# Performance work log

Measured on AMD Instinct MI355X. Metric: run time of the kernel, lower is better.

The kernel has to match this reference:

```python
import jax, jax.numpy as jnp
import numpy as np

N_NODES = 100000
N_EDGES = 1600000
F_IN = 256
F_OUT = 128


def setup_inputs() -> dict:
    key = jax.random.key(0)
    k_x, k_row, k_col, k_v, k_w = jax.random.split(key, 5)
    x = jax.random.normal(k_x, (N_NODES, F_IN), dtype=jnp.float32)
    row = jax.random.randint(k_row, (N_EDGES,), 0, N_NODES, dtype=jnp.int32)
    col = jax.random.randint(k_col, (N_EDGES,), 0, N_NODES, dtype=jnp.int32)
    vals = jax.random.uniform(k_v, (N_EDGES,), dtype=jnp.float32)
    # glorot init for weights_0 [F_IN, F_OUT]
    limit = np.sqrt(6.0 / (F_IN + F_OUT)).astype(np.float32)
    W = jax.random.uniform(k_w, (F_IN, F_OUT), minval=-limit, maxval=limit, dtype=jnp.float32)
    b = jnp.zeros((F_OUT,), dtype=jnp.float32)
    return {"x": x, "W": W, "b": b, "vals": vals, "row": row, "col": col}


def reference(x, W, b, vals, row, col):
    # dropout rate is 0.0 -> identity (tf.nn.dropout(x, keep_prob=1.0))
    pre_sup = x @ W  # [N, F_OUT] dense feature projection
    # SpMM: output[i] = sum_e (vals[e] * pre_sup[col[e]]) for edges with row[e] == i
    msgs = vals[:, None] * pre_sup[col]  # [E, F_OUT] gather + scale
    out = jax.ops.segment_sum(msgs, row, num_segments=N_NODES)  # scatter-add
    return jax.nn.relu(out + b)
```

## Files before the change

### kernel.cpp

```cpp
#include <hip/hip_runtime.h>
#include <hip/hip_bf16.h>

#define N_NODES 100000
#define N_EDGES 1600000
#define F_IN 256
#define F_OUT 128

#define N_BINS 128
#define RPB 782
#define L1_BLOCKS 256
#define L1_THREADS 512
#define L1_EDGES (N_EDGES / L1_BLOCKS)
#define CNT_SIZE (N_BINS * L1_BLOCKS)

typedef __attribute__((ext_vector_type(8))) short short8;
typedef __attribute__((ext_vector_type(4))) float f32x4;
typedef __attribute__((ext_vector_type(2))) float f32x2;
typedef __attribute__((ext_vector_type(2))) unsigned int uint2v;

static __device__ __forceinline__ unsigned short bf16b(float f) {
    __hip_bfloat16 h = __float2bfloat16(f);
    return *reinterpret_cast<unsigned short*>(&h);
}

__global__ void wprep_kernel(const float* __restrict__ W, unsigned short* __restrict__ Wsw) {
    int idx = blockIdx.x * 256 + threadIdx.x;
    int e  = idx & 7;
    int col = (idx >> 3) & 127;
    int kk = (idx >> 10) & 3;
    int ks = idx >> 12;
    int k = ks * 32 + kk * 8 + e;
    Wsw[idx] = bf16b(W[k * 128 + col]);
}

__global__ __launch_bounds__(64) void gemm_kernel(const float* __restrict__ x,
                                                  const unsigned short* __restrict__ Wsw,
                                                  unsigned short* __restrict__ preb) {
    __shared__ char sx[16384];
    const int lane = threadIdx.x;
    const int m0 = blockIdx.x * 16;
    const int l15 = lane & 15;
    const int kk = lane >> 4;

#pragma unroll
    for (int j = 0; j < 16; ++j) {
        const char* gsrc = reinterpret_cast<const char*>(x + (size_t)(m0 + j) * F_IN)
                         + ((lane ^ j) << 4);
        __builtin_amdgcn_global_load_lds(
            (const __attribute__((address_space(1))) void*)gsrc,
            (__attribute__((address_space(3))) void*)(sx + j * 1024),
            16, 0, 0);
    }
    __syncthreads();

    f32x4 acc[8];
#pragma unroll
    for (int i = 0; i < 8; ++i) acc[i] = (f32x4){0.f, 0.f, 0.f, 0.f};

    const char* swb = sx + l15 * 1024;
    const int sw = l15 << 4;
#pragma unroll
    for (int ks = 0; ks < 8; ++ks) {
        const int cb = ks * 128 + kk * 32;
        float4 fa = *reinterpret_cast<const float4*>(swb + ((cb) ^ sw));
        float4 fb = *reinterpret_cast<const float4*>(swb + ((cb + 16) ^ sw));
        short8 a;
        a[0] = (short)bf16b(fa.x); a[1] = (short)bf16b(fa.y);
        a[2] = (short)bf16b(fa.z); a[3] = (short)bf16b(fa.w);
        a[4] = (short)bf16b(fb.x); a[5] = (short)bf16b(fb.y);
        a[6] = (short)bf16b(fb.z); a[7] = (short)bf16b(fb.w);
        const short8* wv = reinterpret_cast<const short8*>(Wsw) + ((ks * 4 + kk) * 128 + l15);
#pragma unroll
        for (int nf = 0; nf < 8; ++nf) {
            short8 b = wv[nf * 16];
            acc[nf] = __builtin_amdgcn_mfma_f32_16x16x32_bf16(a, b, acc[nf], 0, 0, 0);
        }
    }

    const int rbase = m0 + (lane >> 4) * 4;
#pragma unroll
    for (int nf = 0; nf < 8; ++nf) {
        int cc = nf * 16 + l15;
#pragma unroll
        for (int reg = 0; reg < 4; ++reg) {
            preb[(long)(rbase + reg) * F_OUT + cc] = bf16b(acc[nf][reg]);
        }
    }
}

__global__ __launch_bounds__(L1_THREADS) void passA_kernel(const int* __restrict__ row,
                                                           int* __restrict__ cnt) {
    __shared__ int h[N_BINS];
    if (threadIdx.x < N_BINS) h[threadIdx.x] = 0;
    __syncthreads();
    const int g = blockIdx.x;
    const int base = g * L1_EDGES;
    for (int i = threadIdx.x; i < L1_EDGES; i += L1_THREADS) {
        int r = __builtin_nontemporal_load(row + base + i);
        atomicAdd(&h[r / RPB], 1);
    }
    __syncthreads();
    if (threadIdx.x < N_BINS)
        cnt[threadIdx.x * L1_BLOCKS + g] = h[threadIdx.x];
}

__global__ void scan32768_kernel(const int* __restrict__ cnt, int* __restrict__ off) {
    __shared__ int tmp[1024];
    int t = threadIdx.x;
    const int4* c4 = reinterpret_cast<const int4*>(cnt);
    int sum = 0;
#pragma unroll
    for (int j = 0; j < 8; ++j) {
        int4 v = c4[t * 8 + j];
        sum += v.x + v.y + v.z + v.w;
    }
    tmp[t] = sum;
    __syncthreads();
#pragma unroll
    for (int o = 1; o < 1024; o <<= 1) {
        int u = (t >= o) ? tmp[t - o] : 0;
        __syncthreads();
        tmp[t] += u;
        __syncthreads();
    }
    int base = tmp[t] - sum;
#pragma unroll
    for (int j = 0; j < 8; ++j) {
        int4 v = c4[t * 8 + j];
        off[t * 32 + j * 4 + 0] = base; base += v.x;
        off[t * 32 + j * 4 + 1] = base; base += v.y;
        off[t * 32 + j * 4 + 2] = base; base += v.z;
        off[t * 32 + j * 4 + 3] = base; base += v.w;
    }
    if (t == 1023) off[CNT_SIZE] = base;
}

__global__ __launch_bounds__(L1_THREADS) void passB_kernel(const int* __restrict__ row,
                                                           const int* __restrict__ col,
                                                           const float* __restrict__ vals,
                                                           const int* __restrict__ off,
                                                           unsigned* __restrict__ packed,
                                                           unsigned short* __restrict__ valh) {
    __shared__ int cur[N_BINS];
    const int g = blockIdx.x;
    if (threadIdx.x < N_BINS) cur[threadIdx.x] = off[threadIdx.x * L1_BLOCKS + g];
    __syncthreads();
    const int base = g * L1_EDGES;
    for (int i = threadIdx.x; i < L1_EDGES; i += L1_THREADS) {
        int e = base + i;
        int r = __builtin_nontemporal_load(row + e);
        int c = __builtin_nontemporal_load(col + e);
        float v = __builtin_nontemporal_load(vals + e);
        int bin = r / RPB;
        int lr = r - bin * RPB;
        int pos = atomicAdd(&cur[bin], 1);
        packed[pos] = (unsigned)c | ((unsigned)lr << 17);
        valh[pos] = bf16b(v);
    }
}

__global__ __launch_bounds__(1024) void csr_fused_kernel(const unsigned* __restrict__ packed,
                                                         const unsigned short* __restrict__ valh,
                                                         const int* __restrict__ off,
                                                         int* __restrict__ row_start,
                                                         uint2v* __restrict__ edges) {
    __shared__ int tmp[1024];
    const int b = blockIdx.x;
    const int t = threadIdx.x;
    const int rbase = b * RPB;
    const int nrows = min(RPB, N_NODES - rbase);
    const int lo = off[b * L1_BLOCKS];
    const int hi = off[(b + 1) * L1_BLOCKS];

    tmp[t] = 0;
    __syncthreads();
    for (int i = lo + t; i < hi; i += 1024)
        atomicAdd(&tmp[packed[i] >> 17], 1);
    __syncthreads();

    int d = tmp[t];
#pragma unroll
    for (int o = 1; o < 1024; o <<= 1) {
        int u = (t >= o) ? tmp[t - o] : 0;
        __syncthreads();
        tmp[t] += u;
        __syncthreads();
    }
    int excl = lo + tmp[t] - d;
    if (t < nrows) row_start[rbase + t] = excl;
    if (b == N_BINS - 1 && t == 0) row_start[N_NODES] = N_EDGES;
    tmp[t] = excl;
    __syncthreads();

    for (int i = lo + t; i < hi; i += 1024) {
        unsigned p = packed[i];
        unsigned short vh = valh[i];
        int pos = atomicAdd(&tmp[p >> 17], 1);
        edges[pos] = (uint2v){p & 0x1FFFFu, ((unsigned)vh) << 16};
    }
}

__global__ __launch_bounds__(256) void spmm_csr_kernel(
    const unsigned short* __restrict__ preb, const int* __restrict__ row_start,
    const uint2v* __restrict__ edges, const float* __restrict__ bias,
    float* __restrict__ out) {
    const int lane = threadIdx.x & 63;
    const int r = blockIdx.x * 4 + (threadIdx.x >> 6);
    const int s = row_start[r];
    const int t = row_start[r + 1];
    const int n = t - s;
    float a0 = 0.f, a1 = 0.f;

    const char* pb = reinterpret_cast<const char*>(preb);
    const unsigned laneoff = (unsigned)(lane << 2);

    uint2v ev = (uint2v){0u, 0u};
    if (lane < n) ev = edges[s + lane];
    const int nn = n < 64 ? n : 64;
    for (int j0 = 0; j0 < nn; j0 += 8) {
#pragma unroll
        for (int jj = 0; jj < 8; ++jj) {
            int j = j0 + jj;
            unsigned c = (unsigned)__builtin_amdgcn_readlane((int)ev.x, j);
            float v = __uint_as_float((unsigned)__builtin_amdgcn_readlane((int)ev.y, j));
            const char* pbase = pb + ((size_t)c << 8);
            unsigned g = *reinterpret_cast<const unsigned*>(pbase + laneoff);
            a0 += v * __uint_as_float(g << 16);
            a1 += v * __uint_as_float(g & 0xFFFF0000u);
        }
    }
    for (int e = s + 64; e < t; ++e) {
        uint2v cv = edges[e];
        float v = __uint_as_float(cv.y);
        const char* pbase = pb + ((size_t)cv.x << 8);
        unsigned g = *reinterpret_cast<const unsigned*>(pbase + laneoff);
        a0 += v * __uint_as_float(g << 16);
        a1 += v * __uint_as_float(g & 0xFFFF0000u);
    }

    float2 bb = *reinterpret_cast<const float2*>(bias + lane * 2);
    f32x2 o;
    o.x = fmaxf(a0 + bb.x, 0.f);
    o.y = fmaxf(a1 + bb.y, 0.f);
    __builtin_nontemporal_store(o, reinterpret_cast<f32x2*>(out + (size_t)r * F_OUT + lane * 2));
}

extern "C" void kernel_launch(void* const* d_in, const int* in_sizes, int n_in,
                              void* d_out, int out_size, void* d_ws, size_t ws_size,
                              hipStream_t stream) {
    const float* x    = (const float*)d_in[0];
    const float* W    = (const float*)d_in[1];
    const float* b    = (const float*)d_in[2];
    const float* vals = (const float*)d_in[3];
    const int*   row  = (const int*)d_in[4];
    const int*   col  = (const int*)d_in[5];
    float* out = (float*)d_out;

    char* ws = (char*)d_ws;
    unsigned short* preb      = (unsigned short*)(ws);
    unsigned short* Wsw       = (unsigned short*)(ws + 25600000);
    int*            row_start = (int*)(ws + 25665536);
    int*            cnt       = (int*)(ws + 26469664);
    int*            off       = (int*)(ws + 26600736);
    unsigned*       packed    = (unsigned*)(ws + 26731904);
    unsigned short* valh      = (unsigned short*)(ws + 33131904);
    uint2v*         edges     = (uint2v*)(ws + 36331904);

    wprep_kernel<<<128, 256, 0, stream>>>(W, Wsw);
    gemm_kernel<<<N_NODES / 16, 64, 0, stream>>>(x, Wsw, preb);

    passA_kernel<<<L1_BLOCKS, L1_THREADS, 0, stream>>>(row, cnt);
    scan32768_kernel<<<1, 1024, 0, stream>>>(cnt, off);
    passB_kernel<<<L1_BLOCKS, L1_THREADS, 0, stream>>>(row, col, vals, off, packed, valh);

    csr_fused_kernel<<<N_BINS, 1024, 0, stream>>>(packed, valh, off, row_start, edges);

    spmm_csr_kernel<<<N_NODES / 4, 256, 0, stream>>>(preb, row_start, edges, b, out);
}
```

Baseline: 160.6 us.

## Fuse weight prep with histogram and GEMM with scatter into shared launches

Merges the weight bf16 swizzle with the row histogram pass in one launch, and the edge scatter pass with the dense GEMM in another, selecting work by block index. This cuts the kernel count from seven to five and lets the memory-bound scatter overlap with the compute-bound GEMM. Histogram and scatter blocks shrink to 64 threads and their count doubles to 512, so the count array and scan double in size (65536 entries). Atomic contention per block drops, but the single-block scan now handles twice the data and the workspace offsets are repacked.

```diff
diff --git a/kernel.cpp b/kernel.cpp
--- a/kernel.cpp
+++ b/kernel.cpp
@@ -8,8 +8,7 @@
 
 #define N_BINS 128
 #define RPB 782
-#define L1_BLOCKS 256
-#define L1_THREADS 512
+#define L1_BLOCKS 512
 #define L1_EDGES (N_EDGES / L1_BLOCKS)
 #define CNT_SIZE (N_BINS * L1_BLOCKS)
 
@@ -23,22 +22,102 @@
     return *reinterpret_cast<unsigned short*>(&h);
 }
 
-__global__ void wprep_kernel(const float* __restrict__ W, unsigned short* __restrict__ Wsw) {
-    int idx = blockIdx.x * 256 + threadIdx.x;
-    int e  = idx & 7;
-    int col = (idx >> 3) & 127;
-    int kk = (idx >> 10) & 3;
-    int ks = idx >> 12;
-    int k = ks * 32 + kk * 8 + e;
-    Wsw[idx] = bf16b(W[k * 128 + col]);
-}
-
-__global__ __launch_bounds__(64) void gemm_kernel(const float* __restrict__ x,
-                                                  const unsigned short* __restrict__ Wsw,
-                                                  unsigned short* __restrict__ preb) {
-    __shared__ char sx[16384];
-    const int lane = threadIdx.x;
-    const int m0 = blockIdx.x * 16;
+__global__ __launch_bounds__(64) void fuseA_kernel(const float* __restrict__ W,
+                                                   unsigned short* __restrict__ Wsw,
+                                                   const int* __restrict__ row,
+                                                   int* __restrict__ cnt) {
+    const int t = threadIdx.x;
+    if (blockIdx.x < 512) {
+        int idx = blockIdx.x * 64 + t;
+        int e  = idx & 7;
+        int col = (idx >> 3) & 127;
+        int kk = (idx >> 10) & 3;
+        int ks = idx >> 12;
+        int k = ks * 32 + kk * 8 + e;
+        Wsw[idx] = bf16b(W[k * 128 + col]);
+    } else {
+        __shared__ int h[N_BINS];
+        h[t] = 0; h[t + 64] = 0;
+        __syncthreads();
+        const int g = blockIdx.x - 512;
+        const int base = g * L1_EDGES;
+        for (int i = t; i < L1_EDGES; i += 64) {
+            int r = __builtin_nontemporal_load(row + base + i);
+            atomicAdd(&h[r / RPB], 1);
+        }
+        __syncthreads();
+        cnt[t * L1_BLOCKS + g] = h[t];
+        cnt[(t + 64) * L1_BLOCKS + g] = h[t + 64];
+    }
+}
+
+__global__ void scan65536_kernel(const int* __restrict__ cnt, int* __restrict__ off) {
+    __shared__ int tmp[1024];
+    int t = threadIdx.x;
+    const int4* c4 = reinterpret_cast<const int4*>(cnt);
+    int sum = 0;
+#pragma unroll
+    for (int j = 0; j < 16; ++j) {
+        int4 v = c4[t * 16 + j];
+        sum += v.x + v.y + v.z + v.w;
+    }
+    tmp[t] = sum;
+    __syncthreads();
+#pragma unroll
+    for (int o = 1; o < 1024; o <<= 1) {
+        int u = (t >= o) ? tmp[t - o] : 0;
+        __syncthreads();
+        tmp[t] += u;
+        __syncthreads();
+    }
+    int base = tmp[t] - sum;
+#pragma unroll
+    for (int j = 0; j < 16; ++j) {
+        int4 v = c4[t * 16 + j];
+        off[t * 64 + j * 4 + 0] = base; base += v.x;
+        off[t * 64 + j * 4 + 1] = base; base += v.y;
+        off[t * 64 + j * 4 + 2] = base; base += v.z;
+        off[t * 64 + j * 4 + 3] = base; base += v.w;
+    }
+    if (t == 1023) off[CNT_SIZE] = base;
+}
+
+__global__ __launch_bounds__(64) void fuseB_kernel(const int* __restrict__ row,
+                                                   const int* __restrict__ col,
+                                                   const float* __restrict__ vals,
+                                                   const int* __restrict__ off,
+                                                   unsigned* __restrict__ packed,
+                                                   unsigned short* __restrict__ valh,
+                                                   const float* __restrict__ x,
+                                                   const unsigned short* __restrict__ Wsw,
+                                                   unsigned short* __restrict__ preb) {
+    __shared__ char smem[16384];
+    const int t = threadIdx.x;
+
+    if (blockIdx.x < 512) {
+        int* cur = reinterpret_cast<int*>(smem);
+        const int g = blockIdx.x;
+        cur[t] = off[t * L1_BLOCKS + g];
+        cur[t + 64] = off[(t + 64) * L1_BLOCKS + g];
+        __syncthreads();
+        const int base = g * L1_EDGES;
+        for (int i = t; i < L1_EDGES; i += 64) {
+            int e = base + i;
+            int r = __builtin_nontemporal_load(row + e);
+            int c = __builtin_nontemporal_load(col + e);
+            float v = __builtin_nontemporal_load(vals + e);
+            int bin = r / RPB;
+            int lr = r - bin * RPB;
+            int pos = atomicAdd(&cur[bin], 1);
+            packed[pos] = (unsigned)c | ((unsigned)lr << 17);
+            valh[pos] = bf16b(v);
+        }
+        return;
+    }
+
+    char* sx = smem;
+    const int lane = t;
+    const int m0 = (blockIdx.x - 512) * 16;
     const int l15 = lane & 15;
     const int kk = lane >> 4;
 
@@ -85,77 +164,6 @@
         for (int reg = 0; reg < 4; ++reg) {
             preb[(long)(rbase + reg) * F_OUT + cc] = bf16b(acc[nf][reg]);
         }
-    }
-}
-
-__global__ __launch_bounds__(L1_THREADS) void passA_kernel(const int* __restrict__ row,
-                                                           int* __restrict__ cnt) {
-    __shared__ int h[N_BINS];
-    if (threadIdx.x < N_BINS) h[threadIdx.x] = 0;
-    __syncthreads();
-    const int g = blockIdx.x;
-    const int base = g * L1_EDGES;
-    for (int i = threadIdx.x; i < L1_EDGES; i += L1_THREADS) {
-        int r = __builtin_nontemporal_load(row + base + i);
-        atomicAdd(&h[r / RPB], 1);
-    }
-    __syncthreads();
-    if (threadIdx.x < N_BINS)
-        cnt[threadIdx.x * L1_BLOCKS + g] = h[threadIdx.x];
-}
-
-__global__ void scan32768_kernel(const int* __restrict__ cnt, int* __restrict__ off) {
-    __shared__ int tmp[1024];
-    int t = threadIdx.x;
-    const int4* c4 = reinterpret_cast<const int4*>(cnt);
-    int sum = 0;
-#pragma unroll
-    for (int j = 0; j < 8; ++j) {
-        int4 v = c4[t * 8 + j];
-        sum += v.x + v.y + v.z + v.w;
-    }
-    tmp[t] = sum;
-    __syncthreads();
-#pragma unroll
-    for (int o = 1; o < 1024; o <<= 1) {
-        int u = (t >= o) ? tmp[t - o] : 0;
-        __syncthreads();
-        tmp[t] += u;
-        __syncthreads();
-    }
-    int base = tmp[t] - sum;
-#pragma unroll
-    for (int j = 0; j < 8; ++j) {
-        int4 v = c4[t * 8 + j];
-        off[t * 32 + j * 4 + 0] = base; base += v.x;
-        off[t * 32 + j * 4 + 1] = base; base += v.y;
-        off[t * 32 + j * 4 + 2] = base; base += v.z;
-        off[t * 32 + j * 4 + 3] = base; base += v.w;
-    }
-    if (t == 1023) off[CNT_SIZE] = base;
-}
-
-__global__ __launch_bounds__(L1_THREADS) void passB_kernel(const int* __restrict__ row,
-                                                           const int* __restrict__ col,
-                                                           const float* __restrict__ vals,
-                                                           const int* __restrict__ off,
-                                                           unsigned* __restrict__ packed,
-                                                           unsigned short* __restrict__ valh) {
-    __shared__ int cur[N_BINS];
-    const int g = blockIdx.x;
-    if (threadIdx.x < N_BINS) cur[threadIdx.x] = off[threadIdx.x * L1_BLOCKS + g];
-    __syncthreads();
-    const int base = g * L1_EDGES;
-    for (int i = threadIdx.x; i < L1_EDGES; i += L1_THREADS) {
-        int e = base + i;
-        int r = __builtin_nontemporal_load(row + e);
-        int c = __builtin_nontemporal_load(col + e);
-        float v = __builtin_nontemporal_load(vals + e);
-        int bin = r / RPB;
-        int lr = r - bin * RPB;
-        int pos = atomicAdd(&cur[bin], 1);
-        packed[pos] = (unsigned)c | ((unsigned)lr << 17);
-        valh[pos] = bf16b(v);
     }
 }
 
@@ -260,20 +268,16 @@
     unsigned short* preb      = (unsigned short*)(ws);
     unsigned short* Wsw       = (unsigned short*)(ws + 25600000);
     int*            row_start = (int*)(ws + 25665536);
-    int*            cnt       = (int*)(ws + 26469664);
-    int*            off       = (int*)(ws + 26600736);
-    unsigned*       packed    = (unsigned*)(ws + 26731904);
-    unsigned short* valh      = (unsigned short*)(ws + 33131904);
-    uint2v*         edges     = (uint2v*)(ws + 36331904);
-
-    wprep_kernel<<<128, 256, 0, stream>>>(W, Wsw);
-    gemm_kernel<<<N_NODES / 16, 64, 0, stream>>>(x, Wsw, preb);
-
-    passA_kernel<<<L1_BLOCKS, L1_THREADS, 0, stream>>>(row, cnt);
-    scan32768_kernel<<<1, 1024, 0, stream>>>(cnt, off);
-    passB_kernel<<<L1_BLOCKS, L1_THREADS, 0, stream>>>(row, col, vals, off, packed, valh);
-
+    int*            cnt       = (int*)(ws + 26065552);
+    int*            off       = (int*)(ws + 26327696);
+    unsigned*       packed    = (unsigned*)(ws + 26589856);
+    unsigned short* valh      = (unsigned short*)(ws + 32989856);
+    uint2v*         edges     = (uint2v*)(ws + 36189856);
+
+    fuseA_kernel<<<1024, 64, 0, stream>>>(W, Wsw, row, cnt);
+    scan65536_kernel<<<1, 1024, 0, stream>>>(cnt, off);
+    fuseB_kernel<<<512 + N_NODES / 16, 64, 0, stream>>>(row, col, vals, off, packed, valh,
+                                                        x, Wsw, preb);
     csr_fused_kernel<<<N_BINS, 1024, 0, stream>>>(packed, valh, off, row_start, edges);
-
     spmm_csr_kernel<<<N_NODES / 4, 256, 0, stream>>>(preb, row_start, edges, b, out);
 }
```

Result: slower. 213.8 us (+33.2%).

## Fuse W prep, row histogram and x-to-bf16 conversion into one launch; add bf16 GEMM path

Applied to the files above, without the earlier changes.

Merges the weight swizzle, the passA row histogram and a new full conversion of x to bf16 into a single multi-role kernel. When the workspace is large enough, the GEMM then reads the pre-converted bf16 x from a swizzled LDS tile instead of converting fp32 in the inner loop. This removes two launches and halves GEMM input bytes. The cost is an extra full pass that reads x (102MB) and writes 51MB of bf16, which may cost more than it saves.

```diff
diff --git a/kernel.cpp b/kernel.cpp
--- a/kernel.cpp
+++ b/kernel.cpp
@@ -9,9 +9,11 @@
 #define N_BINS 128
 #define RPB 782
 #define L1_BLOCKS 256
-#define L1_THREADS 512
 #define L1_EDGES (N_EDGES / L1_BLOCKS)
 #define CNT_SIZE (N_BINS * L1_BLOCKS)
+
+#define WS_XB16_OFF 49131904ull
+#define WS_NEED_BIG (WS_XB16_OFF + 51200000ull)
 
 typedef __attribute__((ext_vector_type(8))) short short8;
 typedef __attribute__((ext_vector_type(4))) float f32x4;
@@ -23,19 +25,49 @@
     return *reinterpret_cast<unsigned short*>(&h);
 }
 
-__global__ void wprep_kernel(const float* __restrict__ W, unsigned short* __restrict__ Wsw) {
-    int idx = blockIdx.x * 256 + threadIdx.x;
-    int e  = idx & 7;
-    int col = (idx >> 3) & 127;
-    int kk = (idx >> 10) & 3;
-    int ks = idx >> 12;
-    int k = ks * 32 + kk * 8 + e;
-    Wsw[idx] = bf16b(W[k * 128 + col]);
-}
-
-__global__ __launch_bounds__(64) void gemm_kernel(const float* __restrict__ x,
-                                                  const unsigned short* __restrict__ Wsw,
-                                                  unsigned short* __restrict__ preb) {
+__global__ __launch_bounds__(512) void fuseA_kernel(const float* __restrict__ W,
+                                                    unsigned short* __restrict__ Wsw,
+                                                    const int* __restrict__ row,
+                                                    int* __restrict__ cnt,
+                                                    const float* __restrict__ x,
+                                                    unsigned short* __restrict__ xb16) {
+    const int t = threadIdx.x;
+    const unsigned b = blockIdx.x;
+    if (b < 64) {
+        int idx = (int)b * 512 + t;
+        int e  = idx & 7;
+        int col = (idx >> 3) & 127;
+        int kk = (idx >> 10) & 3;
+        int ks = idx >> 12;
+        Wsw[idx] = bf16b(W[(ks * 32 + kk * 8 + e) * 128 + col]);
+    } else if (b < 320) {
+        __shared__ int h[N_BINS];
+        if (t < N_BINS) h[t] = 0;
+        __syncthreads();
+        const int g = (int)b - 64;
+        const int base = g * L1_EDGES;
+        for (int i = t; i < L1_EDGES; i += 512) {
+            int r = __builtin_nontemporal_load(row + base + i);
+            atomicAdd(&h[r / RPB], 1);
+        }
+        __syncthreads();
+        if (t < N_BINS) cnt[t * L1_BLOCKS + g] = h[t];
+    } else {
+        size_t i8 = ((size_t)(b - 320) * 512 + t) * 8;
+        f32x4 a = __builtin_nontemporal_load(reinterpret_cast<const f32x4*>(x + i8));
+        f32x4 c = __builtin_nontemporal_load(reinterpret_cast<const f32x4*>(x + i8 + 4));
+        short8 o;
+        o[0] = (short)bf16b(a.x); o[1] = (short)bf16b(a.y);
+        o[2] = (short)bf16b(a.z); o[3] = (short)bf16b(a.w);
+        o[4] = (short)bf16b(c.x); o[5] = (short)bf16b(c.y);
+        o[6] = (short)bf16b(c.z); o[7] = (short)bf16b(c.w);
+        *reinterpret_cast<short8*>(xb16 + i8) = o;
+    }
+}
+
+__global__ __launch_bounds__(64) void gemm_f32_kernel(const float* __restrict__ x,
+                                                      const unsigned short* __restrict__ Wsw,
+                                                      unsigned short* __restrict__ preb) {
     __shared__ char sx[16384];
     const int lane = threadIdx.x;
     const int m0 = blockIdx.x * 16;
@@ -82,26 +114,58 @@
     for (int nf = 0; nf < 8; ++nf) {
         int cc = nf * 16 + l15;
 #pragma unroll
-        for (int reg = 0; reg < 4; ++reg) {
+        for (int reg = 0; reg < 4; ++reg)
             preb[(long)(rbase + reg) * F_OUT + cc] = bf16b(acc[nf][reg]);
+    }
+}
+
+__global__ __launch_bounds__(64) void gemm_b16_kernel(const unsigned short* __restrict__ xb,
+                                                      const unsigned short* __restrict__ Wsw,
+                                                      unsigned short* __restrict__ preb) {
+    __shared__ char sx[8192];
+    const int lane = threadIdx.x;
+    const int m0 = blockIdx.x * 16;
+    const int l15 = lane & 15;
+    const int kk = lane >> 4;
+
+#pragma unroll
+    for (int j = 0; j < 16; j += 2) {
+        int r = m0 + j + (lane >> 5);
+        int g = lane & 31;
+        const char* gsrc = reinterpret_cast<const char*>(xb + (size_t)r * F_IN)
+                         + ((g ^ (r & 7)) << 4);
+        __builtin_amdgcn_global_load_lds(
+            (const __attribute__((address_space(1))) void*)gsrc,
+            (__attribute__((address_space(3))) void*)(sx + j * 512),
+            16, 0, 0);
+    }
+    __syncthreads();
+
+    f32x4 acc[8];
+#pragma unroll
+    for (int i = 0; i < 8; ++i) acc[i] = (f32x4){0.f, 0.f, 0.f, 0.f};
+
+    const char* swb = sx + l15 * 512;
+    const int r7 = l15 & 7;
+#pragma unroll
+    for (int ks = 0; ks < 8; ++ks) {
+        short8 a = *reinterpret_cast<const short8*>(swb + (((ks * 4 + kk) ^ r7) << 4));
+        const short8* wv = reinterpret_cast<const short8*>(Wsw) + ((ks * 4 + kk) * 128 + l15);
+#pragma unroll
+        for (int nf = 0; nf < 8; ++nf) {
+            short8 b = wv[nf * 16];
+            acc[nf] = __builtin_amdgcn_mfma_f32_16x16x32_bf16(a, b, acc[nf], 0, 0, 0);
         }
     }
-}
-
-__global__ __launch_bounds__(L1_THREADS) void passA_kernel(const int* __restrict__ row,
-                                                           int* __restrict__ cnt) {
-    __shared__ int h[N_BINS];
-    if (threadIdx.x < N_BINS) h[threadIdx.x] = 0;
-    __syncthreads();
-    const int g = blockIdx.x;
-    const int base = g * L1_EDGES;
-    for (int i = threadIdx.x; i < L1_EDGES; i += L1_THREADS) {
-        int r = __builtin_nontemporal_load(row + base + i);
-        atomicAdd(&h[r / RPB], 1);
-    }
-    __syncthreads();
-    if (threadIdx.x < N_BINS)
-        cnt[threadIdx.x * L1_BLOCKS + g] = h[threadIdx.x];
+
+    const int rbase = m0 + (lane >> 4) * 4;
+#pragma unroll
+    for (int nf = 0; nf < 8; ++nf) {
+        int cc = nf * 16 + l15;
+#pragma unroll
+        for (int reg = 0; reg < 4; ++reg)
+            preb[(long)(rbase + reg) * F_OUT + cc] = bf16b(acc[nf][reg]);
+    }
 }
 
 __global__ void scan32768_kernel(const int* __restrict__ cnt, int* __restrict__ off) {
@@ -135,18 +199,18 @@
     if (t == 1023) off[CNT_SIZE] = base;
 }
 
-__global__ __launch_bounds__(L1_THREADS) void passB_kernel(const int* __restrict__ row,
-                                                           const int* __restrict__ col,
-                                                           const float* __restrict__ vals,
-                                                           const int* __restrict__ off,
-                                                           unsigned* __restrict__ packed,
-                                                           unsigned short* __restrict__ valh) {
+__global__ __launch_bounds__(512) void passB_kernel(const int* __restrict__ row,
+                                                    const int* __restrict__ col,
+                                                    const float* __restrict__ vals,
+                                                    const int* __restrict__ off,
+                                                    unsigned* __restrict__ packed,
+                                                    unsigned short* __restrict__ valh) {
     __shared__ int cur[N_BINS];
     const int g = blockIdx.x;
     if (threadIdx.x < N_BINS) cur[threadIdx.x] = off[threadIdx.x * L1_BLOCKS + g];
     __syncthreads();
     const int base = g * L1_EDGES;
-    for (int i = threadIdx.x; i < L1_EDGES; i += L1_THREADS) {
+    for (int i = threadIdx.x; i < L1_EDGES; i += 512) {
         int e = base + i;
         int r = __builtin_nontemporal_load(row + e);
         int c = __builtin_nontemporal_load(col + e);
@@ -265,15 +329,18 @@
     unsigned*       packed    = (unsigned*)(ws + 26731904);
     unsigned short* valh      = (unsigned short*)(ws + 33131904);
     uint2v*         edges     = (uint2v*)(ws + 36331904);
-
-    wprep_kernel<<<128, 256, 0, stream>>>(W, Wsw);
-    gemm_kernel<<<N_NODES / 16, 64, 0, stream>>>(x, Wsw, preb);
-
-    passA_kernel<<<L1_BLOCKS, L1_THREADS, 0, stream>>>(row, cnt);
+    unsigned short* xb16      = (unsigned short*)(ws + WS_XB16_OFF);
+
+    const bool big = (ws_size >= WS_NEED_BIG);
+
+    fuseA_kernel<<<big ? 6570 : 320, 512, 0, stream>>>(W, Wsw, row, cnt, x, xb16);
+    if (big)
+        gemm_b16_kernel<<<N_NODES / 16, 64, 0, stream>>>(xb16, Wsw, preb);
+    else
+        gemm_f32_kernel<<<N_NODES / 16, 64, 0, stream>>>(x, Wsw, preb);
+
     scan32768_kernel<<<1, 1024, 0, stream>>>(cnt, off);
-    passB_kernel<<<L1_BLOCKS, L1_THREADS, 0, stream>>>(row, col, vals, off, packed, valh);
-
+    passB_kernel<<<L1_BLOCKS, 512, 0, stream>>>(row, col, vals, off, packed, valh);
     csr_fused_kernel<<<N_BINS, 1024, 0, stream>>>(packed, valh, off, row_start, edges);
-
     spmm_csr_kernel<<<N_NODES / 4, 256, 0, stream>>>(preb, row_start, edges, b, out);
 }
```

New measurement: 170.9 us. 1.06x slower.
